# Kernel optimization log

Measured on AMD Instinct MI355X. Metric: run time of the kernel, lower is better.

The kernel has to match this reference:

```python
import jax, jax.numpy as jnp
import numpy as np

N = 8192
BOX = 50.0
CUTOFF = 5.0
MAX_E = 64 * N  # padded edge capacity (~34 avg neighbors expected)


def setup_inputs() -> dict:
    key = jax.random.key(0)
    pos = jax.random.uniform(key, (N, 3), dtype=jnp.float32) * BOX
    return {"pos": pos}


def _pairwise_dist(pos):
    # Euclidean cdist via the gram-matrix identity; avoids the [N,N,3] intermediate.
    sq = jnp.sum(pos * pos, axis=-1)                      # [N]
    d2 = sq[:, None] + sq[None, :] - 2.0 * (pos @ pos.T)  # [N,N]
    return jnp.sqrt(jnp.maximum(d2, 0.0))


def reference(pos):
    n = pos.shape[0]
    dist = _pairwise_dist(pos)
    # mask self-edges by pushing the diagonal above the cutoff (as in the torch code)
    dist = dist + (CUTOFF + 1.0) * jnp.eye(n, dtype=dist.dtype)
    mask = dist < CUTOFF
    # data-dependent nonzero -> fixed-size padded output for jit compatibility;
    # padded entries are filled with -1.
    rows, cols = jnp.nonzero(mask, size=MAX_E, fill_value=-1)
    return jnp.stack([rows, cols], axis=0)  # [2, MAX_E], int32
```

## Files before the change

### kernel.cpp

```cpp
#include <hip/hip_runtime.h>
#include <stdint.h>

#define N 8192
#define MAX_E (64 * N)
#define NCHUNK (N / 64)
#define TILE 2048
#define CTILES (N / TILE)
#define CPAIRS (TILE / 128)
#define ROWS_PER_WAVE 8
#define WAVES 4
#define ROWS_PER_BLOCK (ROWS_PER_WAVE * WAVES)
#define RGROUPS (N / ROWS_PER_BLOCK)

__device__ __forceinline__ float sq_exact(float x, float y, float z) {
    return __fadd_rn(__fadd_rn(__fmul_rn(x, x), __fmul_rn(y, y)), __fmul_rn(z, z));
}

__device__ __forceinline__ bool edge_pred(float xi, float yi, float zi, float sqi,
                                          const float4& pj) {
    float dot = __fmaf_rn(zi, pj.z, __fmaf_rn(yi, pj.y, __fmul_rn(xi, pj.x)));
    float d2  = __fmaf_rn(-2.0f, dot, __fadd_rn(sqi, pj.w));
    return d2 < 0x1.8ffffep+4f;
}

__global__ __launch_bounds__(256) void mask_kernel(const float* __restrict__ posf,
                                                   uint64_t* __restrict__ masks,
                                                   int* __restrict__ counts4) {
    __shared__ float4 pts[TILE];
    const int tid  = threadIdx.x;
    const int wave = tid >> 6;
    const int lane = tid & 63;
    const int row0 = blockIdx.x * ROWS_PER_BLOCK + wave * ROWS_PER_WAVE;
    const int ct   = blockIdx.y;
    const int cb   = ct * TILE;

    float xi[ROWS_PER_WAVE], yi[ROWS_PER_WAVE], zi[ROWS_PER_WAVE], sqi[ROWS_PER_WAVE];
    uint64_t k0[ROWS_PER_WAVE], k1[ROWS_PER_WAVE];
#pragma unroll
    for (int r = 0; r < ROWS_PER_WAVE; r++) {
        int i = row0 + r;
        xi[r] = posf[3 * i + 0];
        yi[r] = posf[3 * i + 1];
        zi[r] = posf[3 * i + 2];
        sqi[r] = sq_exact(xi[r], yi[r], zi[r]);
        k0[r] = 0; k1[r] = 0;
    }

    for (int k = tid; k < TILE; k += 256) {
        float x = posf[3 * (cb + k) + 0];
        float y = posf[3 * (cb + k) + 1];
        float z = posf[3 * (cb + k) + 2];
        pts[k] = make_float4(x, y, z, sq_exact(x, y, z));
    }
    __syncthreads();

    float4 pa = pts[lane];
    float4 pb = pts[64 + lane];
#pragma unroll
    for (int c = 0; c < TILE; c += 128) {
        float4 na = pts[((c + 128) & (TILE - 1)) + lane];
        float4 nb = pts[((c + 192) & (TILE - 1)) + lane];
        const int owner = c >> 7;
#pragma unroll
        for (int r = 0; r < ROWS_PER_WAVE; r++) {
            uint64_t ma = __ballot(edge_pred(xi[r], yi[r], zi[r], sqi[r], pa));
            if (lane == owner) k0[r] = ma;
            uint64_t mb = __ballot(edge_pred(xi[r], yi[r], zi[r], sqi[r], pb));
            if (lane == owner) k1[r] = mb;
        }
        pa = na; pb = nb;
    }

#pragma unroll
    for (int r = 0; r < ROWS_PER_WAVE; r++) {
        const int row = row0 + r;
        if ((row >> 11) == ct) {
            const int ls = (row & (TILE - 1)) >> 6;
            if (lane == (ls >> 1)) {
                uint64_t clr = ~(1ull << (row & 63));
                if (ls & 1) k1[r] &= clr; else k0[r] &= clr;
            }
        }
        if (lane < CPAIRS) {
            ulonglong2 v; v.x = k0[r]; v.y = k1[r];
            ((ulonglong2*)(masks + (size_t)row * NCHUNK))[ct * CPAIRS + lane] = v;
        }
        int t = __popcll(k0[r]) + __popcll(k1[r]);
#pragma unroll
        for (int o = 32; o > 0; o >>= 1) t += __shfl_down(t, o);
        if (lane == 0) counts4[row * CTILES + ct] = t;
    }
}

__global__ __launch_bounds__(256) void scan_kernel(const int* __restrict__ counts4,
                                                   int* __restrict__ offsets) {
    __shared__ int part[256];
    const int t = threadIdx.x;
    int local[32];
    int s = 0;
#pragma unroll
    for (int k = 0; k < 32; k++) {
        int v = 0;
#pragma unroll
        for (int j = 0; j < CTILES; j++) v += counts4[(t * 32 + k) * CTILES + j];
        local[k] = v; s += v;
    }
    part[t] = s;
    __syncthreads();
    for (int off = 1; off < 256; off <<= 1) {
        int v = (t >= off) ? part[t - off] : 0;
        __syncthreads();
        part[t] += v;
        __syncthreads();
    }
    int run = (t > 0) ? part[t - 1] : 0;
#pragma unroll
    for (int k = 0; k < 32; k++) { offsets[t * 32 + k] = run; run += local[k]; }
    if (t == 255) offsets[N] = part[255];
}

__global__ __launch_bounds__(256) void emit_kernel(const uint64_t* __restrict__ masks,
                                                   const int* __restrict__ offsets,
                                                   int* __restrict__ out) {
    const int wave = threadIdx.x >> 6;
    const int lane = threadIdx.x & 63;
    const int row  = blockIdx.x * 4 + wave;

    {
        const int E = offsets[N];
        const int idx = E + blockIdx.x * 256 + threadIdx.x;
        if (idx < MAX_E) { out[idx] = -1; out[MAX_E + idx] = -1; }
    }

    ulonglong2 v = ((const ulonglong2*)(masks + (size_t)row * NCHUNK))[lane];
    int s0 = __popcll(v.x), s1 = __popcll(v.y);
    int x = s0 + s1;
#pragma unroll
    for (int o = 1; o < 64; o <<= 1) {
        int t = __shfl_up(x, o);
        if (lane >= o) x += t;
    }
    int slot = offsets[row] + (x - (s0 + s1));

    const int col0 = lane * 128;
    uint64_t m = v.x;
    while (m) {
        int b = __ffsll((unsigned long long)m) - 1;
        m &= m - 1;
        if (slot < MAX_E) { out[slot] = row; out[MAX_E + slot] = col0 + b; }
        slot++;
    }
    m = v.y;
    while (m) {
        int b = __ffsll((unsigned long long)m) - 1;
        m &= m - 1;
        if (slot < MAX_E) { out[slot] = row; out[MAX_E + slot] = col0 + 64 + b; }
        slot++;
    }
}

extern "C" void kernel_launch(void* const* d_in, const int* in_sizes, int n_in,
                              void* d_out, int out_size, void* d_ws, size_t ws_size,
                              hipStream_t stream) {
    const float* posf = (const float*)d_in[0];
    int* out = (int*)d_out;
    int* counts4 = (int*)d_ws;
    int* offsets = (int*)((char*)d_ws + (256 << 10));
    uint64_t* masks = (uint64_t*)((char*)d_ws + (512 << 10));

    dim3 grid(RGROUPS, CTILES);
    mask_kernel<<<grid, 256, 0, stream>>>(posf, masks, counts4);
    scan_kernel<<<1, 256, 0, stream>>>(counts4, offsets);
    emit_kernel<<<N / 4, 256, 0, stream>>>(masks, offsets, out);
}
```

Baseline: 87.43 us.

## Fuse scan into emit kernel with redundant per-block prefix sums

Removes the single-block scan kernel and its launch. Each of 512 emit blocks now redoes the full 8192-row prefix sum from counts4 (vectorised int4 loads) and derives offsets for its own 16 rows, then emits 4 rows per wave and fills the padding with a grid-stride loop. The mask kernel's column loop is changed from full unroll to unroll 4. This drops one launch and the serial single-block dependency, at the cost of redundant counts reads in every block.

After: 91.19 us. +4.3%, slower.

```diff
diff --git a/kernel.cpp b/kernel.cpp
--- a/kernel.cpp
+++ b/kernel.cpp
@@ -11,6 +11,8 @@
 #define WAVES 4
 #define ROWS_PER_BLOCK (ROWS_PER_WAVE * WAVES)
 #define RGROUPS (N / ROWS_PER_BLOCK)
+#define E_BLOCKS 512
+#define E_ROWS 16
 
 __device__ __forceinline__ float sq_exact(float x, float y, float z) {
     return __fadd_rn(__fadd_rn(__fmul_rn(x, x), __fmul_rn(y, y)), __fmul_rn(z, z));
@@ -56,7 +58,7 @@
 
     float4 pa = pts[lane];
     float4 pb = pts[64 + lane];
-#pragma unroll
+#pragma unroll 4
     for (int c = 0; c < TILE; c += 128) {
         float4 na = pts[((c + 128) & (TILE - 1)) + lane];
         float4 nb = pts[((c + 192) & (TILE - 1)) + lane];
@@ -92,70 +94,79 @@
     }
 }
 
-__global__ __launch_bounds__(256) void scan_kernel(const int* __restrict__ counts4,
-                                                   int* __restrict__ offsets) {
+__global__ __launch_bounds__(256) void emit_kernel(const uint64_t* __restrict__ masks,
+                                                   const int* __restrict__ counts4,
+                                                   int* __restrict__ out) {
+    const int tid  = threadIdx.x;
+    const int wave = tid >> 6;
+    const int lane = tid & 63;
+    const int row0 = blockIdx.x * E_ROWS;
+
     __shared__ int part[256];
-    const int t = threadIdx.x;
-    int local[32];
+    __shared__ int roff[E_ROWS];
+    __shared__ int Etot_s;
+
+    const int4* c4 = (const int4*)counts4;
     int s = 0;
-#pragma unroll
+#pragma unroll 8
     for (int k = 0; k < 32; k++) {
-        int v = 0;
-#pragma unroll
-        for (int j = 0; j < CTILES; j++) v += counts4[(t * 32 + k) * CTILES + j];
-        local[k] = v; s += v;
+        int4 v = c4[tid * 32 + k];
+        s += v.x + v.y + v.z + v.w;
     }
-    part[t] = s;
+    part[tid] = s;
     __syncthreads();
     for (int off = 1; off < 256; off <<= 1) {
-        int v = (t >= off) ? part[t - off] : 0;
+        int v = (tid >= off) ? part[tid - off] : 0;
         __syncthreads();
-        part[t] += v;
+        part[tid] += v;
         __syncthreads();
     }
-    int run = (t > 0) ? part[t - 1] : 0;
-#pragma unroll
-    for (int k = 0; k < 32; k++) { offsets[t * 32 + k] = run; run += local[k]; }
-    if (t == 255) offsets[N] = part[255];
-}
+    if (tid < E_ROWS) {
+        const int ch = row0 >> 5;
+        int off = (ch > 0) ? part[ch - 1] : 0;
+        for (int rr = (ch << 5); rr < row0 + tid; rr++) {
+            int4 v = c4[rr];
+            off += v.x + v.y + v.z + v.w;
+        }
+        roff[tid] = off;
+    }
+    if (tid == 0) Etot_s = part[255];
+    __syncthreads();
 
-__global__ __launch_bounds__(256) void emit_kernel(const uint64_t* __restrict__ masks,
-                                                   const int* __restrict__ offsets,
-                                                   int* __restrict__ out) {
-    const int wave = threadIdx.x >> 6;
-    const int lane = threadIdx.x & 63;
-    const int row  = blockIdx.x * 4 + wave;
-
-    {
-        const int E = offsets[N];
-        const int idx = E + blockIdx.x * 256 + threadIdx.x;
-        if (idx < MAX_E) { out[idx] = -1; out[MAX_E + idx] = -1; }
+    const int E = Etot_s;
+    for (int idx = E + blockIdx.x * 256 + tid; idx < MAX_E; idx += E_BLOCKS * 256) {
+        out[idx] = -1; out[MAX_E + idx] = -1;
     }
 
-    ulonglong2 v = ((const ulonglong2*)(masks + (size_t)row * NCHUNK))[lane];
-    int s0 = __popcll(v.x), s1 = __popcll(v.y);
-    int x = s0 + s1;
 #pragma unroll
-    for (int o = 1; o < 64; o <<= 1) {
-        int t = __shfl_up(x, o);
-        if (lane >= o) x += t;
-    }
-    int slot = offsets[row] + (x - (s0 + s1));
+    for (int r = 0; r < 4; r++) {
+        const int lr  = wave * 4 + r;
+        const int row = row0 + lr;
+        ulonglong2 v = ((const ulonglong2*)(masks + (size_t)row * NCHUNK))[lane];
+        int s0 = __popcll(v.x), s1 = __popcll(v.y);
+        int x = s0 + s1;
+#pragma unroll
+        for (int o = 1; o < 64; o <<= 1) {
+            int t = __shfl_up(x, o);
+            if (lane >= o) x += t;
+        }
+        int slot = roff[lr] + (x - (s0 + s1));
 
-    const int col0 = lane * 128;
-    uint64_t m = v.x;
-    while (m) {
-        int b = __ffsll((unsigned long long)m) - 1;
-        m &= m - 1;
-        if (slot < MAX_E) { out[slot] = row; out[MAX_E + slot] = col0 + b; }
-        slot++;
-    }
-    m = v.y;
-    while (m) {
-        int b = __ffsll((unsigned long long)m) - 1;
-        m &= m - 1;
-        if (slot < MAX_E) { out[slot] = row; out[MAX_E + slot] = col0 + 64 + b; }
-        slot++;
+        const int col0 = lane * 128;
+        uint64_t m = v.x;
+        while (m) {
+            int b = __ffsll((unsigned long long)m) - 1;
+            m &= m - 1;
+            if (slot < MAX_E) { out[slot] = row; out[MAX_E + slot] = col0 + b; }
+            slot++;
+        }
+        m = v.y;
+        while (m) {
+            int b = __ffsll((unsigned long long)m) - 1;
+            m &= m - 1;
+            if (slot < MAX_E) { out[slot] = row; out[MAX_E + slot] = col0 + 64 + b; }
+            slot++;
+        }
     }
 }
 
@@ -165,11 +176,9 @@
     const float* posf = (const float*)d_in[0];
     int* out = (int*)d_out;
     int* counts4 = (int*)d_ws;
-    int* offsets = (int*)((char*)d_ws + (256 << 10));
     uint64_t* masks = (uint64_t*)((char*)d_ws + (512 << 10));
 
     dim3 grid(RGROUPS, CTILES);
     mask_kernel<<<grid, 256, 0, stream>>>(posf, masks, counts4);
-    scan_kernel<<<1, 256, 0, stream>>>(counts4, offsets);
-    emit_kernel<<<N / 4, 256, 0, stream>>>(masks, offsets, out);
+    emit_kernel<<<E_BLOCKS, 256, 0, stream>>>(masks, counts4, out);
 }
```
